# Performance work log

Measured on AMD Instinct MI355X. Metric: run time of the kernel, lower is better.

The kernel has to match this reference:

```python
import jax, jax.numpy as jnp
import numpy as np

N_NODES = 100000
N_EDGES = 1600000
IN_DIM = 128
HID = 32
HEADS = 4
OUT_DIM = 40
NEG_SLOPE = 0.2
BN_EPS = 1e-5


def setup_inputs() -> dict:
    key = jax.random.key(0)
    ks = jax.random.split(key, 13)
    x = jax.random.normal(ks[0], (N_NODES, IN_DIM), jnp.float32)
    edge_index = jax.random.randint(ks[1], (2, N_EDGES), 0, N_NODES, dtype=jnp.int32)
    s0 = 1.0 / np.sqrt(IN_DIM)
    s1 = 1.0 / np.sqrt(HEADS * HID)
    return {
        "x": x,
        "edge_index": edge_index,
        # layer 0: GATConv(IN_DIM -> HID, HEADS heads, concat)
        "W0": jax.random.normal(ks[2], (IN_DIM, HEADS * HID), jnp.float32) * s0,
        "a_src0": jax.random.normal(ks[3], (HEADS, HID), jnp.float32) * s0,
        "a_dst0": jax.random.normal(ks[4], (HEADS, HID), jnp.float32) * s0,
        "b0": jnp.zeros((HEADS * HID,), jnp.float32),
        # BatchNorm1d(HEADS*HID)
        "gamma0": jnp.ones((HEADS * HID,), jnp.float32),
        "beta0": jnp.zeros((HEADS * HID,), jnp.float32),
        # layer 1: GATConv(HEADS*HID -> OUT_DIM, 1 head, mean)
        "W1": jax.random.normal(ks[5], (HEADS * HID, OUT_DIM), jnp.float32) * s1,
        "a_src1": jax.random.normal(ks[6], (1, OUT_DIM), jnp.float32) * s1,
        "a_dst1": jax.random.normal(ks[7], (1, OUT_DIM), jnp.float32) * s1,
        "b1": jnp.zeros((OUT_DIM,), jnp.float32),
    }


def gat_conv(x, src, dst, n_nodes, W, a_src, a_dst, b, heads, concat):
    # linear transform: [N, H, C]
    h = (x @ W).reshape(n_nodes, heads, -1)
    # per-node attention logits [N, H]
    alpha_src = (h * a_src).sum(-1)
    alpha_dst = (h * a_dst).sum(-1)
    # per-edge raw attention [E, H]
    e = jax.nn.leaky_relu(alpha_src[src] + alpha_dst[dst], NEG_SLOPE)
    # softmax over incoming edges of each destination node
    m = jax.ops.segment_max(e, dst, num_segments=n_nodes)  # self-loops -> no empty segment
    ex = jnp.exp(e - m[dst])
    den = jax.ops.segment_sum(ex, dst, num_segments=n_nodes)
    # weighted scatter-aggregate of messages [E, H, C] -> [N, H, C]
    out = jax.ops.segment_sum(ex[:, :, None] * h[src], dst, num_segments=n_nodes)
    out = out / den[:, :, None]
    out = out.reshape(n_nodes, -1) if concat else out.mean(axis=1)
    return out + b


def batch_norm(x, gamma, beta):
    mu = x.mean(axis=0)
    var = x.var(axis=0)
    return (x - mu) * jax.lax.rsqrt(var + BN_EPS) * gamma + beta


def reference(x, edge_index, W0, a_src0, a_dst0, b0, gamma0, beta0,
              W1, a_src1, a_dst1, b1):
    n = x.shape[0]
    loop = jnp.arange(n, dtype=edge_index.dtype)
    src = jnp.concatenate([edge_index[0], loop])  # add self-loops (PyG default)
    dst = jnp.concatenate([edge_index[1], loop])
    # layer 0: GATConv -> BN -> ELU (dropout p=0 / eval -> identity)
    h = gat_conv(x, src, dst, n, W0, a_src0, a_dst0, b0, HEADS, True)
    h = jax.nn.elu(batch_norm(h, gamma0, beta0))
    # layer 1: GATConv, 1 head, mean aggregation, no BN/act
    out = gat_conv(h, src, dst, n, W1, a_src1, a_dst1, b1, 1, False)
    return out
```

## Files before the change

kernel.cpp:

```cpp
#include <hip/hip_runtime.h>
#include <hip/hip_bf16.h>
#include <math.h>

#define NN   100000
#define EE   1600000
#define ETOT (NN + EE)
#define IND  128
#define HD   128
#define OD   40
#define NEG  0.2f
#define BNEPS 1e-5f

typedef __attribute__((ext_vector_type(8))) short bf16x8;
typedef __attribute__((ext_vector_type(4))) float f32x4;

__device__ __forceinline__ float lrelu(float x) { return x > 0.f ? x : NEG * x; }

__device__ __forceinline__ unsigned pack_bf16(float a, float b) {
  unsigned ua = __float_as_uint(a), ub = __float_as_uint(b);
  ua = (ua + 0x7fffu + ((ua >> 16) & 1u)) >> 16;
  ub = (ub + 0x7fffu + ((ub >> 16) & 1u)) >> 16;
  return ua | (ub << 16);
}
__device__ __forceinline__ float bf16_lo(unsigned v) { return __uint_as_float(v << 16); }
__device__ __forceinline__ float bf16_hi(unsigned v) { return __uint_as_float(v & 0xffff0000u); }

__global__ __launch_bounds__(256) void w0pack_kernel(const float* __restrict__ W0,
                                                     unsigned* __restrict__ w0t) {
  int idx = blockIdx.x * 256 + threadIdx.x;
  if (idx >= 128 * 64) return;
  int n = idx & 127, kp = idx >> 7;
  float lo = W0[(size_t)(2 * kp) * 128 + n];
  float hi = W0[(size_t)(2 * kp + 1) * 128 + n];
  w0t[n * 64 + kp] = pack_bf16(lo, hi);
}

__global__ __launch_bounds__(256) void gemm0_kernel(const float* __restrict__ x,
                                                    const unsigned* __restrict__ w0t,
                                                    const float* __restrict__ a_src0,
                                                    const float* __restrict__ a_dst0,
                                                    unsigned* __restrict__ h0b,
                                                    float* __restrict__ asrc0,
                                                    float* __restrict__ adst0) {
  __shared__ __align__(16) unsigned As[64][68];
  __shared__ __align__(16) unsigned Wt[128][68];
  int t = threadIdx.x;
  int rowbase = blockIdx.x * 64;
  for (int idx = t; idx < 128 * 64; idx += 256) {
    Wt[idx >> 6][idx & 63] = w0t[idx];
  }
  for (int idx = t; idx < 64 * 64; idx += 256) {
    int row = idx >> 6, kp = idx & 63;
    int r = rowbase + row;
    int rc = r < NN ? r : NN - 1;
    float2 v = *(const float2*)&x[(size_t)rc * 128 + kp * 2];
    As[row][kp] = pack_bf16(v.x, v.y);
  }
  __syncthreads();

  int lane = t & 63, w = t >> 6;
  int mrow = lane & 15, g = lane >> 4;
  f32x4 acc[8];
#pragma unroll
  for (int nt = 0; nt < 8; nt++) acc[nt] = (f32x4){0.f, 0.f, 0.f, 0.f};
#pragma unroll
  for (int ks = 0; ks < 4; ks++) {
    bf16x8 a = *(const bf16x8*)&As[w * 16 + mrow][ks * 16 + g * 4];
#pragma unroll
    for (int nt = 0; nt < 8; nt++) {
      bf16x8 b = *(const bf16x8*)&Wt[nt * 16 + mrow][ks * 16 + g * 4];
      acc[nt] = __builtin_amdgcn_mfma_f32_16x16x32_bf16(a, b, acc[nt], 0, 0, 0);
    }
  }
  int col = lane & 15;
  float as_[8], ad_[8];
#pragma unroll
  for (int nt = 0; nt < 8; nt++) {
    as_[nt] = a_src0[nt * 16 + col];
    ad_[nt] = a_dst0[nt * 16 + col];
  }
#pragma unroll
  for (int reg = 0; reg < 4; reg++) {
    int r = rowbase + w * 16 + g * 4 + reg;
    bool rok = r < NN;
    float hs0 = acc[0][reg] * as_[0] + acc[1][reg] * as_[1];
    float hs1 = acc[2][reg] * as_[2] + acc[3][reg] * as_[3];
    float hs2 = acc[4][reg] * as_[4] + acc[5][reg] * as_[5];
    float hs3 = acc[6][reg] * as_[6] + acc[7][reg] * as_[7];
    float hd0 = acc[0][reg] * ad_[0] + acc[1][reg] * ad_[1];
    float hd1 = acc[2][reg] * ad_[2] + acc[3][reg] * ad_[3];
    float hd2 = acc[4][reg] * ad_[4] + acc[5][reg] * ad_[5];
    float hd3 = acc[6][reg] * ad_[6] + acc[7][reg] * ad_[7];
#pragma unroll
    for (int mk = 1; mk < 16; mk <<= 1) {
      hs0 += __shfl_xor(hs0, mk); hs1 += __shfl_xor(hs1, mk);
      hs2 += __shfl_xor(hs2, mk); hs3 += __shfl_xor(hs3, mk);
      hd0 += __shfl_xor(hd0, mk); hd1 += __shfl_xor(hd1, mk);
      hd2 += __shfl_xor(hd2, mk); hd3 += __shfl_xor(hd3, mk);
    }
    if ((lane & 15) == 0 && rok) {
      asrc0[r * 4 + 0] = hs0; asrc0[r * 4 + 1] = hs1;
      asrc0[r * 4 + 2] = hs2; asrc0[r * 4 + 3] = hs3;
      adst0[r * 4 + 0] = hd0; adst0[r * 4 + 1] = hd1;
      adst0[r * 4 + 2] = hd2; adst0[r * 4 + 3] = hd3;
    }
#pragma unroll
    for (int nt = 0; nt < 8; nt++) {
      float v = acc[nt][reg];
      float nv = __shfl_xor(v, 1);
      if (!(col & 1) && rok) h0b[(size_t)r * 64 + nt * 8 + (col >> 1)] = pack_bf16(v, nv);
    }
  }
}

__global__ void degrank_kernel(const int* __restrict__ ei, int* __restrict__ deg,
                               int* __restrict__ rank) {
  int i = blockIdx.x * blockDim.x + threadIdx.x;
  if (i >= ETOT) return;
  int dst = (i < EE) ? ei[EE + i] : (i - EE);
  rank[i] = atomicAdd(&deg[dst], 1);
}

__global__ __launch_bounds__(256) void scanA_kernel(const int* __restrict__ deg,
                                                    int* __restrict__ scanned,
                                                    int* __restrict__ blocksums) {
  __shared__ int s[256];
  int t = threadIdx.x;
  int i = blockIdx.x * 256 + t;
  int v = (i < NN) ? deg[i] : 0;
  s[t] = v;
  __syncthreads();
  for (int off = 1; off < 256; off <<= 1) {
    int add = (t >= off) ? s[t - off] : 0;
    __syncthreads();
    s[t] += add;
    __syncthreads();
  }
  if (i < NN) scanned[i] = s[t];
  if (t == 255) blocksums[blockIdx.x] = s[255];
}

__global__ __launch_bounds__(512) void scanB_kernel(int* __restrict__ blocksums, int NB) {
  __shared__ int s[512];
  int t = threadIdx.x;
  int v = (t < NB) ? blocksums[t] : 0;
  s[t] = v;
  __syncthreads();
  for (int off = 1; off < 512; off <<= 1) {
    int add = (t >= off) ? s[t - off] : 0;
    __syncthreads();
    s[t] += add;
    __syncthreads();
  }
  if (t < NB) blocksums[t] = s[t] - v;
}

__global__ __launch_bounds__(256) void scanC_kernel(const int* __restrict__ scanned,
                                                    const int* __restrict__ deg,
                                                    const int* __restrict__ blocksums,
                                                    int* __restrict__ rowptr) {
  int i = blockIdx.x * 256 + threadIdx.x;
  if (i < NN) rowptr[i] = blocksums[blockIdx.x] + scanned[i] - deg[i];
  if (i == 0) rowptr[NN] = ETOT;
}

__global__ void scatter_kernel(const int* __restrict__ ei, const int* __restrict__ rowptr,
                               const int* __restrict__ rank, int* __restrict__ csr_src) {
  int i = blockIdx.x * blockDim.x + threadIdx.x;
  if (i >= ETOT) return;
  int src, dst;
  if (i < EE) { src = ei[i]; dst = ei[EE + i]; }
  else        { src = dst = i - EE; }
  csr_src[rowptr[dst] + rank[i]] = src;
}

__global__ __launch_bounds__(256) void agg0_kernel(const int* __restrict__ csr_src,
                                                   const int* __restrict__ rowptr,
                                                   const float* __restrict__ asrc0,
                                                   const float* __restrict__ adst0,
                                                   const unsigned* __restrict__ h0b,
                                                   const float* __restrict__ b0,
                                                   float* __restrict__ agg0) {
  __shared__ float ws[4][4][72];
  __shared__ int   ss[4][64];
  int t = threadIdx.x;
  int lane = t & 63, wv = t >> 6;
  int n = blockIdx.x * 4 + wv;
  if (n >= NN) return;
  int start = rowptr[n], end = rowptr[n + 1];
  float4 ad = *(const float4*)&adst0[(size_t)n * 4];
  int q = lane >> 4, cp = lane & 15;
  int head = cp >> 2;
  float a0 = 0.f, a1 = 0.f, a2 = 0.f, a3 = 0.f, a4 = 0.f, a5 = 0.f, a6 = 0.f, a7 = 0.f;
  float d0 = 0.f, d1 = 0.f, d2 = 0.f, d3 = 0.f;

  for (int base = start; base < end; base += 64) {
    int cnt = min(64, end - base);
    if (lane < cnt) {
      int s = csr_src[base + lane];
      float4 as = *(const float4*)&asrc0[(size_t)s * 4];
      float w0 = __expf(lrelu(as.x + ad.x));
      float w1 = __expf(lrelu(as.y + ad.y));
      float w2 = __expf(lrelu(as.z + ad.z));
      float w3 = __expf(lrelu(as.w + ad.w));
      d0 += w0; d1 += w1; d2 += w2; d3 += w3;
      ss[wv][lane] = s;
      ws[wv][0][lane] = w0;
      ws[wv][1][lane] = w1;
      ws[wv][2][lane] = w2;
      ws[wv][3][lane] = w3;
    }
    __builtin_amdgcn_wave_barrier();
    for (int eb = 0; eb < cnt; eb += 4) {
      int e = eb + q;
      float w = (e < cnt) ? ws[wv][head][e] : 0.f;
      int ec = (e < cnt) ? e : cnt - 1;
      int s = ss[wv][ec];
      uint4 hv = *(const uint4*)&h0b[(size_t)s * 64 + cp * 4];
      a0 += w * bf16_lo(hv.x); a1 += w * bf16_hi(hv.x);
      a2 += w * bf16_lo(hv.y); a3 += w * bf16_hi(hv.y);
      a4 += w * bf16_lo(hv.z); a5 += w * bf16_hi(hv.z);
      a6 += w * bf16_lo(hv.w); a7 += w * bf16_hi(hv.w);
    }
    __builtin_amdgcn_wave_barrier();
  }
#pragma unroll
  for (int mk = 1; mk < 64; mk <<= 1) {
    d0 += __shfl_xor(d0, mk);
    d1 += __shfl_xor(d1, mk);
    d2 += __shfl_xor(d2, mk);
    d3 += __shfl_xor(d3, mk);
  }
  a0 += __shfl_xor(a0, 16); a1 += __shfl_xor(a1, 16);
  a2 += __shfl_xor(a2, 16); a3 += __shfl_xor(a3, 16);
  a4 += __shfl_xor(a4, 16); a5 += __shfl_xor(a5, 16);
  a6 += __shfl_xor(a6, 16); a7 += __shfl_xor(a7, 16);
  a0 += __shfl_xor(a0, 32); a1 += __shfl_xor(a1, 32);
  a2 += __shfl_xor(a2, 32); a3 += __shfl_xor(a3, 32);
  a4 += __shfl_xor(a4, 32); a5 += __shfl_xor(a5, 32);
  a6 += __shfl_xor(a6, 32); a7 += __shfl_xor(a7, 32);
  if (q == 0) {
    float dh = head == 0 ? d0 : head == 1 ? d1 : head == 2 ? d2 : d3;
    float rd = 1.f / dh;
    int c = cp * 8;
    float4 o1, o2;
    o1.x = a0 * rd + b0[c + 0]; o1.y = a1 * rd + b0[c + 1];
    o1.z = a2 * rd + b0[c + 2]; o1.w = a3 * rd + b0[c + 3];
    o2.x = a4 * rd + b0[c + 4]; o2.y = a5 * rd + b0[c + 5];
    o2.z = a6 * rd + b0[c + 6]; o2.w = a7 * rd + b0[c + 7];
    *(float4*)&agg0[(size_t)n * 128 + c] = o1;
    *(float4*)&agg0[(size_t)n * 128 + c + 4] = o2;
  }
}

__global__ __launch_bounds__(256) void bnstats_kernel(const float* __restrict__ agg0,
                                                      float* __restrict__ bnsum,
                                                      float* __restrict__ bnsq) {
  int t = threadIdx.x;
  int c = t & 127;
  int g = blockIdx.x * 2 + (t >> 7);
  float s = 0.f, q = 0.f;
  for (int r = g; r < NN; r += 1024) {
    float v = agg0[(size_t)r * 128 + c];
    s += v;
    q += v * v;
  }
  __shared__ float ls[256], lq[256];
  ls[t] = s; lq[t] = q;
  __syncthreads();
  if (t < 128) {
    s = ls[t] + ls[t + 128];
    q = lq[t] + lq[t + 128];
    atomicAdd(&bnsum[c], s);
    atomicAdd(&bnsq[c], q);
  }
}

__global__ void bnfinal_kernel(const float* __restrict__ bnsum, const float* __restrict__ bnsq,
                               const float* __restrict__ gamma, const float* __restrict__ beta,
                               float* __restrict__ bnscale, float* __restrict__ bnshift) {
  int c = threadIdx.x;
  float mu = bnsum[c] / (float)NN;
  float var = bnsq[c] / (float)NN - mu * mu;
  float sc = gamma[c] / sqrtf(var + BNEPS);
  bnscale[c] = sc;
  bnshift[c] = beta[c] - mu * sc;
}

__global__ __launch_bounds__(256) void gemm1_kernel(const float* __restrict__ agg0,
                                                    const float* __restrict__ bnscale,
                                                    const float* __restrict__ bnshift,
                                                    const float* __restrict__ W1,
                                                    const float* __restrict__ a_src1,
                                                    const float* __restrict__ a_dst1,
                                                    unsigned* __restrict__ h1b,
                                                    float* __restrict__ asrc1,
                                                    float* __restrict__ adst1) {
  __shared__ __align__(16) unsigned As[64][68];
  __shared__ __align__(16) unsigned Wt[48][68];
  int t = threadIdx.x;
  int rowbase = blockIdx.x * 64;

  for (int idx = t; idx < 48 * 64; idx += 256) {
    int c = idx >> 6, kp = idx & 63;
    float lo = (c < OD) ? W1[(size_t)(2 * kp) * OD + c] : 0.f;
    float hi = (c < OD) ? W1[(size_t)(2 * kp + 1) * OD + c] : 0.f;
    Wt[c][kp] = pack_bf16(lo, hi);
  }
  for (int idx = t; idx < 64 * 32; idx += 256) {
    int row = idx >> 5, k4 = idx & 31;
    int r = rowbase + row;
    int rc = r < NN ? r : NN - 1;
    int k = k4 * 4;
    float4 v  = *(const float4*)&agg0[(size_t)rc * 128 + k];
    float4 sc = *(const float4*)&bnscale[k];
    float4 sh = *(const float4*)&bnshift[k];
    float y0 = v.x * sc.x + sh.x;
    float y1 = v.y * sc.y + sh.y;
    float y2 = v.z * sc.z + sh.z;
    float y3 = v.w * sc.w + sh.w;
    y0 = y0 > 0.f ? y0 : expm1f(y0);
    y1 = y1 > 0.f ? y1 : expm1f(y1);
    y2 = y2 > 0.f ? y2 : expm1f(y2);
    y3 = y3 > 0.f ? y3 : expm1f(y3);
    As[row][k4 * 2]     = pack_bf16(y0, y1);
    As[row][k4 * 2 + 1] = pack_bf16(y2, y3);
  }
  __syncthreads();

  int lane = t & 63, w = t >> 6;
  int mrow = lane & 15, g = lane >> 4;
  f32x4 acc0 = {0.f, 0.f, 0.f, 0.f};
  f32x4 acc1 = {0.f, 0.f, 0.f, 0.f};
  f32x4 acc2 = {0.f, 0.f, 0.f, 0.f};
#pragma unroll
  for (int ks = 0; ks < 4; ks++) {
    bf16x8 a = *(const bf16x8*)&As[w * 16 + mrow][ks * 16 + g * 4];
    bf16x8 b0v = *(const bf16x8*)&Wt[mrow][ks * 16 + g * 4];
    bf16x8 b1v = *(const bf16x8*)&Wt[16 + mrow][ks * 16 + g * 4];
    bf16x8 b2v = *(const bf16x8*)&Wt[32 + mrow][ks * 16 + g * 4];
    acc0 = __builtin_amdgcn_mfma_f32_16x16x32_bf16(a, b0v, acc0, 0, 0, 0);
    acc1 = __builtin_amdgcn_mfma_f32_16x16x32_bf16(a, b1v, acc1, 0, 0, 0);
    acc2 = __builtin_amdgcn_mfma_f32_16x16x32_bf16(a, b2v, acc2, 0, 0, 0);
  }
  int col = lane & 15;
  float as0 = (col < OD)      ? a_src1[col]      : 0.f;
  float as1 = (16 + col < OD) ? a_src1[16 + col] : 0.f;
  float as2 = (32 + col < OD) ? a_src1[32 + col] : 0.f;
  float ad0 = (col < OD)      ? a_dst1[col]      : 0.f;
  float ad1 = (16 + col < OD) ? a_dst1[16 + col] : 0.f;
  float ad2 = (32 + col < OD) ? a_dst1[32 + col] : 0.f;
#pragma unroll
  for (int reg = 0; reg < 4; reg++) {
    int r = rowbase + w * 16 + g * 4 + reg;
    float v0 = acc0[reg], v1 = acc1[reg], v2 = acc2[reg];
    float ps = v0 * as0 + v1 * as1 + v2 * as2;
    float pd = v0 * ad0 + v1 * ad1 + v2 * ad2;
#pragma unroll
    for (int mk = 1; mk < 16; mk <<= 1) { ps += __shfl_xor(ps, mk); pd += __shfl_xor(pd, mk); }
    bool rok = r < NN;
    if ((lane & 15) == 0 && rok) { asrc1[r] = ps; adst1[r] = pd; }
    float n0 = __shfl_xor(v0, 1), n1 = __shfl_xor(v1, 1), n2 = __shfl_xor(v2, 1);
    if (!(col & 1) && rok) {
      h1b[(size_t)r * 20 + ((col) >> 1)]      = pack_bf16(v0, n0);
      h1b[(size_t)r * 20 + ((16 + col) >> 1)] = pack_bf16(v1, n1);
      if (32 + col < OD) h1b[(size_t)r * 20 + ((32 + col) >> 1)] = pack_bf16(v2, n2);
    }
  }
}

__global__ __launch_bounds__(256) void agg1_kernel(const int* __restrict__ csr_src,
                                                   const int* __restrict__ rowptr,
                                                   const float* __restrict__ asrc1,
                                                   const float* __restrict__ adst1,
                                                   const unsigned* __restrict__ h1b,
                                                   const float* __restrict__ b1,
                                                   float* __restrict__ out) {
  __shared__ float ws[4][64];
  __shared__ int   ss[4][64];
  int t = threadIdx.x;
  int lane = t & 63, wv = t >> 6;
  int n = blockIdx.x * 4 + wv;
  if (n >= NN) return;
  int start = rowptr[n], end = rowptr[n + 1];
  float ad = adst1[n];
  int esub = lane / 20;
  int chan = lane - esub * 20;
  float dsum = 0.f, acc0 = 0.f, acc1 = 0.f;
  for (int base = start; base < end; base += 64) {
    int cnt = min(64, end - base);
    if (lane < cnt) {
      int s = csr_src[base + lane];
      float w = __expf(lrelu(asrc1[s] + ad));
      dsum += w;
      ss[wv][lane] = s;
      ws[wv][lane] = w;
    }
    __builtin_amdgcn_wave_barrier();
    if (lane < 60) {
      for (int e = esub; e < cnt; e += 3) {
        int s = ss[wv][e];
        float w = ws[wv][e];
        unsigned hv = h1b[(size_t)s * 20 + chan];
        acc0 += w * bf16_lo(hv);
        acc1 += w * bf16_hi(hv);
      }
    }
    __builtin_amdgcn_wave_barrier();
  }
#pragma unroll
  for (int mk = 1; mk < 64; mk <<= 1) dsum += __shfl_xor(dsum, mk);
  float rd = 1.f / dsum;
  float b0v = __shfl(acc0, lane + 20);
  float c0v = __shfl(acc0, lane + 40);
  float b1v = __shfl(acc1, lane + 20);
  float c1v = __shfl(acc1, lane + 40);
  if (lane < 20) {
    float2 o;
    o.x = (acc0 + b0v + c0v) * rd + b1[lane * 2];
    o.y = (acc1 + b1v + c1v) * rd + b1[lane * 2 + 1];
    *(float2*)&out[(size_t)n * 40 + lane * 2] = o;
  }
}

extern "C" void kernel_launch(void* const* d_in, const int* in_sizes, int n_in,
                              void* d_out, int out_size, void* d_ws, size_t ws_size,
                              hipStream_t stream) {
  const float* x       = (const float*)d_in[0];
  const int*   ei      = (const int*)d_in[1];
  const float* W0      = (const float*)d_in[2];
  const float* a_src0  = (const float*)d_in[3];
  const float* a_dst0  = (const float*)d_in[4];
  const float* b0      = (const float*)d_in[5];
  const float* gamma0  = (const float*)d_in[6];
  const float* beta0   = (const float*)d_in[7];
  const float* W1      = (const float*)d_in[8];
  const float* a_src1  = (const float*)d_in[9];
  const float* a_dst1  = (const float*)d_in[10];
  const float* b1      = (const float*)d_in[11];
  float* out = (float*)d_out;

  char* ws = (char*)d_ws;
  size_t off = 0;
  auto alloc = [&](size_t bytes) {
    void* p = ws + off;
    off += (bytes + 255) & ~(size_t)255;
    return p;
  };
  int*   deg      = (int*)alloc((size_t)NN * 4);
  float* bnsum    = (float*)alloc(128 * 4);
  float* bnsq     = (float*)alloc(128 * 4);
  unsigned* h0b   = (unsigned*)alloc((size_t)NN * 64 * 4);
  float* agg0     = (float*)alloc((size_t)NN * 128 * 4);
  unsigned* h1b   = (unsigned*)alloc((size_t)NN * 20 * 4);
  float* asrc0    = (float*)alloc((size_t)NN * 4 * 4);
  float* adst0    = (float*)alloc((size_t)NN * 4 * 4);
  float* asrc1    = (float*)alloc((size_t)NN * 4);
  float* adst1    = (float*)alloc((size_t)NN * 4);
  float* bnscale  = (float*)alloc(128 * 4);
  float* bnshift  = (float*)alloc(128 * 4);
  int*   rowptr   = (int*)alloc((size_t)(NN + 1) * 4);
  int*   scanned  = (int*)alloc((size_t)NN * 4);
  int*   csr      = (int*)alloc((size_t)ETOT * 4);
  int*   rank     = (int*)alloc((size_t)ETOT * 4);
  int*   bsums    = (int*)alloc(512 * 4);
  unsigned* w0t   = (unsigned*)alloc(128 * 64 * 4);
  (void)ws_size; (void)in_sizes; (void)n_in; (void)out_size;

  size_t zbytes = (char*)(bnsq + 128) - (char*)deg;
  hipMemsetAsync(deg, 0, zbytes, stream);

  const int NB = (NN + 255) / 256;
  const int egrid = (ETOT + 255) / 256;

  w0pack_kernel<<<32, 256, 0, stream>>>(W0, w0t);
  gemm0_kernel<<<(NN + 63) / 64, 256, 0, stream>>>(x, w0t, a_src0, a_dst0, h0b, asrc0, adst0);
  degrank_kernel<<<egrid, 256, 0, stream>>>(ei, deg, rank);
  scanA_kernel<<<NB, 256, 0, stream>>>(deg, scanned, bsums);
  scanB_kernel<<<1, 512, 0, stream>>>(bsums, NB);
  scanC_kernel<<<NB, 256, 0, stream>>>(scanned, deg, bsums, rowptr);
  scatter_kernel<<<egrid, 256, 0, stream>>>(ei, rowptr, rank, csr);
  agg0_kernel<<<(NN + 3) / 4, 256, 0, stream>>>(csr, rowptr, asrc0, adst0, h0b, b0, agg0);
  bnstats_kernel<<<512, 256, 0, stream>>>(agg0, bnsum, bnsq);
  bnfinal_kernel<<<1, 128, 0, stream>>>(bnsum, bnsq, gamma0, beta0, bnscale, bnshift);
  gemm1_kernel<<<(NN + 63) / 64, 256, 0, stream>>>(agg0, bnscale, bnshift, W1, a_src1, a_dst1,
                                                   h1b, asrc1, adst1);
  agg1_kernel<<<(NN + 3) / 4, 256, 0, stream>>>(csr, rowptr, asrc1, adst1, h1b, b1, out);
}
```

Measured before the change: 346.9 us.

## Store layer-0 aggregate in bf16 and map one node per 16-lane group

The layer-0 aggregation kernel now assigns each destination node to a 16-thread group instead of a full 64-lane wave. Each lane handles 8 channels and processes four edges per iteration with independent gathers. This drops the cross-quarter shuffle reduction and the lanes left idle on low-degree nodes. The aggregate is written as packed bf16 rather than fp32, which halves traffic for the BN stats and gemm1 reads, at the cost of extra rounding before batch-norm statistics.

```diff
diff --git a/kernel.cpp b/kernel.cpp
--- a/kernel.cpp
+++ b/kernel.cpp
@@ -180,99 +180,119 @@
                                                    const float* __restrict__ adst0,
                                                    const unsigned* __restrict__ h0b,
                                                    const float* __restrict__ b0,
-                                                   float* __restrict__ agg0) {
-  __shared__ float ws[4][4][72];
-  __shared__ int   ss[4][64];
-  int t = threadIdx.x;
-  int lane = t & 63, wv = t >> 6;
-  int n = blockIdx.x * 4 + wv;
+                                                   unsigned* __restrict__ agg0b) {
+  __shared__ float ws[16][4][17];
+  __shared__ int   ss[16][16];
+  int t = threadIdx.x;
+  int grp = t >> 4;
+  int p   = t & 15;
+  int n = blockIdx.x * 16 + grp;
   if (n >= NN) return;
   int start = rowptr[n], end = rowptr[n + 1];
   float4 ad = *(const float4*)&adst0[(size_t)n * 4];
-  int q = lane >> 4, cp = lane & 15;
-  int head = cp >> 2;
+  int head = p >> 2;
   float a0 = 0.f, a1 = 0.f, a2 = 0.f, a3 = 0.f, a4 = 0.f, a5 = 0.f, a6 = 0.f, a7 = 0.f;
   float d0 = 0.f, d1 = 0.f, d2 = 0.f, d3 = 0.f;
 
-  for (int base = start; base < end; base += 64) {
-    int cnt = min(64, end - base);
-    if (lane < cnt) {
-      int s = csr_src[base + lane];
+  for (int base = start; base < end; base += 16) {
+    int cnt = min(16, end - base);
+    if (p < cnt) {
+      int s = csr_src[base + p];
       float4 as = *(const float4*)&asrc0[(size_t)s * 4];
       float w0 = __expf(lrelu(as.x + ad.x));
       float w1 = __expf(lrelu(as.y + ad.y));
       float w2 = __expf(lrelu(as.z + ad.z));
       float w3 = __expf(lrelu(as.w + ad.w));
       d0 += w0; d1 += w1; d2 += w2; d3 += w3;
-      ss[wv][lane] = s;
-      ws[wv][0][lane] = w0;
-      ws[wv][1][lane] = w1;
-      ws[wv][2][lane] = w2;
-      ws[wv][3][lane] = w3;
+      ss[grp][p] = s;
+      ws[grp][0][p] = w0;
+      ws[grp][1][p] = w1;
+      ws[grp][2][p] = w2;
+      ws[grp][3][p] = w3;
     }
     __builtin_amdgcn_wave_barrier();
     for (int eb = 0; eb < cnt; eb += 4) {
-      int e = eb + q;
-      float w = (e < cnt) ? ws[wv][head][e] : 0.f;
-      int ec = (e < cnt) ? e : cnt - 1;
-      int s = ss[wv][ec];
-      uint4 hv = *(const uint4*)&h0b[(size_t)s * 64 + cp * 4];
-      a0 += w * bf16_lo(hv.x); a1 += w * bf16_hi(hv.x);
-      a2 += w * bf16_lo(hv.y); a3 += w * bf16_hi(hv.y);
-      a4 += w * bf16_lo(hv.z); a5 += w * bf16_hi(hv.z);
-      a6 += w * bf16_lo(hv.w); a7 += w * bf16_hi(hv.w);
+      int e0 = eb, e1 = eb + 1, e2 = eb + 2, e3 = eb + 3;
+      float w0 = ws[grp][head][e0];
+      float w1 = (e1 < cnt) ? ws[grp][head][e1] : 0.f;
+      float w2 = (e2 < cnt) ? ws[grp][head][e2] : 0.f;
+      float w3 = (e3 < cnt) ? ws[grp][head][e3] : 0.f;
+      int s0 = ss[grp][e0];
+      int s1 = ss[grp][(e1 < cnt) ? e1 : e0];
+      int s2 = ss[grp][(e2 < cnt) ? e2 : e0];
+      int s3 = ss[grp][(e3 < cnt) ? e3 : e0];
+      uint4 h0v = *(const uint4*)&h0b[(size_t)s0 * 64 + p * 4];
+      uint4 h1v = *(const uint4*)&h0b[(size_t)s1 * 64 + p * 4];
+      uint4 h2v = *(const uint4*)&h0b[(size_t)s2 * 64 + p * 4];
+      uint4 h3v = *(const uint4*)&h0b[(size_t)s3 * 64 + p * 4];
+      a0 += w0 * bf16_lo(h0v.x); a1 += w0 * bf16_hi(h0v.x);
+      a2 += w0 * bf16_lo(h0v.y); a3 += w0 * bf16_hi(h0v.y);
+      a4 += w0 * bf16_lo(h0v.z); a5 += w0 * bf16_hi(h0v.z);
+      a6 += w0 * bf16_lo(h0v.w); a7 += w0 * bf16_hi(h0v.w);
+      a0 += w1 * bf16_lo(h1v.x); a1 += w1 * bf16_hi(h1v.x);
+      a2 += w1 * bf16_lo(h1v.y); a3 += w1 * bf16_hi(h1v.y);
+      a4 += w1 * bf16_lo(h1v.z); a5 += w1 * bf16_hi(h1v.z);
+      a6 += w1 * bf16_lo(h1v.w); a7 += w1 * bf16_hi(h1v.w);
+      a0 += w2 * bf16_lo(h2v.x); a1 += w2 * bf16_hi(h2v.x);
+      a2 += w2 * bf16_lo(h2v.y); a3 += w2 * bf16_hi(h2v.y);
+      a4 += w2 * bf16_lo(h2v.z); a5 += w2 * bf16_hi(h2v.z);
+      a6 += w2 * bf16_lo(h2v.w); a7 += w2 * bf16_hi(h2v.w);
+      a0 += w3 * bf16_lo(h3v.x); a1 += w3 * bf16_hi(h3v.x);
+      a2 += w3 * bf16_lo(h3v.y); a3 += w3 * bf16_hi(h3v.y);
+      a4 += w3 * bf16_lo(h3v.z); a5 += w3 * bf16_hi(h3v.z);
+      a6 += w3 * bf16_lo(h3v.w); a7 += w3 * bf16_hi(h3v.w);
     }
     __builtin_amdgcn_wave_barrier();
   }
 #pragma unroll
-  for (int mk = 1; mk < 64; mk <<= 1) {
+  for (int mk = 1; mk < 16; mk <<= 1) {
     d0 += __shfl_xor(d0, mk);
     d1 += __shfl_xor(d1, mk);
     d2 += __shfl_xor(d2, mk);
     d3 += __shfl_xor(d3, mk);
   }
-  a0 += __shfl_xor(a0, 16); a1 += __shfl_xor(a1, 16);
-  a2 += __shfl_xor(a2, 16); a3 += __shfl_xor(a3, 16);
-  a4 += __shfl_xor(a4, 16); a5 += __shfl_xor(a5, 16);
-  a6 += __shfl_xor(a6, 16); a7 += __shfl_xor(a7, 16);
-  a0 += __shfl_xor(a0, 32); a1 += __shfl_xor(a1, 32);
-  a2 += __shfl_xor(a2, 32); a3 += __shfl_xor(a3, 32);
-  a4 += __shfl_xor(a4, 32); a5 += __shfl_xor(a5, 32);
-  a6 += __shfl_xor(a6, 32); a7 += __shfl_xor(a7, 32);
-  if (q == 0) {
-    float dh = head == 0 ? d0 : head == 1 ? d1 : head == 2 ? d2 : d3;
-    float rd = 1.f / dh;
-    int c = cp * 8;
-    float4 o1, o2;
-    o1.x = a0 * rd + b0[c + 0]; o1.y = a1 * rd + b0[c + 1];
-    o1.z = a2 * rd + b0[c + 2]; o1.w = a3 * rd + b0[c + 3];
-    o2.x = a4 * rd + b0[c + 4]; o2.y = a5 * rd + b0[c + 5];
-    o2.z = a6 * rd + b0[c + 6]; o2.w = a7 * rd + b0[c + 7];
-    *(float4*)&agg0[(size_t)n * 128 + c] = o1;
-    *(float4*)&agg0[(size_t)n * 128 + c + 4] = o2;
-  }
-}
-
-__global__ __launch_bounds__(256) void bnstats_kernel(const float* __restrict__ agg0,
+  float dh = head == 0 ? d0 : head == 1 ? d1 : head == 2 ? d2 : d3;
+  float rd = 1.f / dh;
+  int c = p * 8;
+  float4 b1v = *(const float4*)&b0[c];
+  float4 b2v = *(const float4*)&b0[c + 4];
+  float o0 = a0 * rd + b1v.x, o1 = a1 * rd + b1v.y;
+  float o2 = a2 * rd + b1v.z, o3 = a3 * rd + b1v.w;
+  float o4 = a4 * rd + b2v.x, o5 = a5 * rd + b2v.y;
+  float o6 = a6 * rd + b2v.z, o7 = a7 * rd + b2v.w;
+  uint4 o;
+  o.x = pack_bf16(o0, o1);
+  o.y = pack_bf16(o2, o3);
+  o.z = pack_bf16(o4, o5);
+  o.w = pack_bf16(o6, o7);
+  *(uint4*)&agg0b[(size_t)n * 64 + p * 4] = o;
+}
+
+__global__ __launch_bounds__(256) void bnstats_kernel(const unsigned* __restrict__ agg0b,
                                                       float* __restrict__ bnsum,
                                                       float* __restrict__ bnsq) {
   int t = threadIdx.x;
-  int c = t & 127;
-  int g = blockIdx.x * 2 + (t >> 7);
-  float s = 0.f, q = 0.f;
-  for (int r = g; r < NN; r += 1024) {
-    float v = agg0[(size_t)r * 128 + c];
-    s += v;
-    q += v * v;
-  }
-  __shared__ float ls[256], lq[256];
-  ls[t] = s; lq[t] = q;
+  int c2 = t & 63;
+  int rg = t >> 6;
+  float sl = 0.f, sh = 0.f, ql = 0.f, qh = 0.f;
+  for (int r = blockIdx.x * 4 + rg; r < NN; r += 2048) {
+    unsigned u = agg0b[(size_t)r * 64 + c2];
+    float lo = bf16_lo(u), hi = bf16_hi(u);
+    sl += lo; sh += hi;
+    ql += lo * lo; qh += hi * hi;
+  }
+  __shared__ float L1[256], L2[256], L3[256], L4[256];
+  L1[t] = sl; L2[t] = sh; L3[t] = ql; L4[t] = qh;
   __syncthreads();
-  if (t < 128) {
-    s = ls[t] + ls[t + 128];
-    q = lq[t] + lq[t + 128];
-    atomicAdd(&bnsum[c], s);
-    atomicAdd(&bnsq[c], q);
+  if (t < 64) {
+    sl = L1[t] + L1[t + 64] + L1[t + 128] + L1[t + 192];
+    sh = L2[t] + L2[t + 64] + L2[t + 128] + L2[t + 192];
+    ql = L3[t] + L3[t + 64] + L3[t + 128] + L3[t + 192];
+    qh = L4[t] + L4[t + 64] + L4[t + 128] + L4[t + 192];
+    atomicAdd(&bnsum[2 * t], sl);
+    atomicAdd(&bnsum[2 * t + 1], sh);
+    atomicAdd(&bnsq[2 * t], ql);
+    atomicAdd(&bnsq[2 * t + 1], qh);
   }
 }
 
@@ -287,7 +307,7 @@
   bnshift[c] = beta[c] - mu * sc;
 }
 
-__global__ __launch_bounds__(256) void gemm1_kernel(const float* __restrict__ agg0,
+__global__ __launch_bounds__(256) void gemm1_kernel(const unsigned* __restrict__ agg0b,
                                                     const float* __restrict__ bnscale,
                                                     const float* __restrict__ bnshift,
                                                     const float* __restrict__ W1,
@@ -307,24 +327,36 @@
     float hi = (c < OD) ? W1[(size_t)(2 * kp + 1) * OD + c] : 0.f;
     Wt[c][kp] = pack_bf16(lo, hi);
   }
-  for (int idx = t; idx < 64 * 32; idx += 256) {
-    int row = idx >> 5, k4 = idx & 31;
+  for (int idx = t; idx < 64 * 16; idx += 256) {
+    int row = idx >> 4, c4 = idx & 15;
     int r = rowbase + row;
     int rc = r < NN ? r : NN - 1;
-    int k = k4 * 4;
-    float4 v  = *(const float4*)&agg0[(size_t)rc * 128 + k];
-    float4 sc = *(const float4*)&bnscale[k];
-    float4 sh = *(const float4*)&bnshift[k];
-    float y0 = v.x * sc.x + sh.x;
-    float y1 = v.y * sc.y + sh.y;
-    float y2 = v.z * sc.z + sh.z;
-    float y3 = v.w * sc.w + sh.w;
+    int k = c4 * 8;
+    uint4 hv = *(const uint4*)&agg0b[(size_t)rc * 64 + c4 * 4];
+    float4 sc1 = *(const float4*)&bnscale[k];
+    float4 sc2 = *(const float4*)&bnscale[k + 4];
+    float4 sh1 = *(const float4*)&bnshift[k];
+    float4 sh2 = *(const float4*)&bnshift[k + 4];
+    float y0 = bf16_lo(hv.x) * sc1.x + sh1.x;
+    float y1 = bf16_hi(hv.x) * sc1.y + sh1.y;
+    float y2 = bf16_lo(hv.y) * sc1.z + sh1.z;
+    float y3 = bf16_hi(hv.y) * sc1.w + sh1.w;
+    float y4 = bf16_lo(hv.z) * sc2.x + sh2.x;
+    float y5 = bf16_hi(hv.z) * sc2.y + sh2.y;
+    float y6 = bf16_lo(hv.w) * sc2.z + sh2.z;
+    float y7 = bf16_hi(hv.w) * sc2.w + sh2.w;
     y0 = y0 > 0.f ? y0 : expm1f(y0);
     y1 = y1 > 0.f ? y1 : expm1f(y1);
     y2 = y2 > 0.f ? y2 : expm1f(y2);
     y3 = y3 > 0.f ? y3 : expm1f(y3);
-    As[row][k4 * 2]     = pack_bf16(y0, y1);
-    As[row][k4 * 2 + 1] = pack_bf16(y2, y3);
+    y4 = y4 > 0.f ? y4 : expm1f(y4);
+    y5 = y5 > 0.f ? y5 : expm1f(y5);
+    y6 = y6 > 0.f ? y6 : expm1f(y6);
+    y7 = y7 > 0.f ? y7 : expm1f(y7);
+    As[row][c4 * 4 + 0] = pack_bf16(y0, y1);
+    As[row][c4 * 4 + 1] = pack_bf16(y2, y3);
+    As[row][c4 * 4 + 2] = pack_bf16(y4, y5);
+    As[row][c4 * 4 + 3] = pack_bf16(y6, y7);
   }
   __syncthreads();
 
@@ -451,7 +483,7 @@
   float* bnsum    = (float*)alloc(128 * 4);
   float* bnsq     = (float*)alloc(128 * 4);
   unsigned* h0b   = (unsigned*)alloc((size_t)NN * 64 * 4);
-  float* agg0     = (float*)alloc((size_t)NN * 128 * 4);
+  unsigned* agg0b = (unsigned*)alloc((size_t)NN * 64 * 4);
   unsigned* h1b   = (unsigned*)alloc((size_t)NN * 20 * 4);
   float* asrc0    = (float*)alloc((size_t)NN * 4 * 4);
   float* adst0    = (float*)alloc((size_t)NN * 4 * 4);
@@ -480,10 +512,10 @@
   scanB_kernel<<<1, 512, 0, stream>>>(bsums, NB);
   scanC_kernel<<<NB, 256, 0, stream>>>(scanned, deg, bsums, rowptr);
   scatter_kernel<<<egrid, 256, 0, stream>>>(ei, rowptr, rank, csr);
-  agg0_kernel<<<(NN + 3) / 4, 256, 0, stream>>>(csr, rowptr, asrc0, adst0, h0b, b0, agg0);
-  bnstats_kernel<<<512, 256, 0, stream>>>(agg0, bnsum, bnsq);
+  agg0_kernel<<<(NN + 15) / 16, 256, 0, stream>>>(csr, rowptr, asrc0, adst0, h0b, b0, agg0b);
+  bnstats_kernel<<<512, 256, 0, stream>>>(agg0b, bnsum, bnsq);
   bnfinal_kernel<<<1, 128, 0, stream>>>(bnsum, bnsq, gamma0, beta0, bnscale, bnshift);
-  gemm1_kernel<<<(NN + 63) / 64, 256, 0, stream>>>(agg0, bnscale, bnshift, W1, a_src1, a_dst1,
+  gemm1_kernel<<<(NN + 63) / 64, 256, 0, stream>>>(agg0b, bnscale, bnshift, W1, a_src1, a_dst1,
                                                    h1b, asrc1, adst1);
   agg1_kernel<<<(NN + 3) / 4, 256, 0, stream>>>(csr, rowptr, asrc1, adst1, h1b, b1, out);
 }
```

Result: faster. 339.9 us (-2.0%).
